# Performance work log

Measured on AMD Instinct MI355X. Metric: run time of the kernel, lower is better.

The kernel has to match this reference:

```python
import jax, jax.numpy as jnp
import numpy as np

S = 7  # adaptive max-pool output size (output_size init kwarg)


def setup_inputs() -> dict:
    key = jax.random.key(0)
    k1, k2, k3, k4, k5, k6 = jax.random.split(key, 6)
    N, C, H, W, R = 4, 256, 50, 50, 256
    images = jax.random.normal(k1, (N, C, H, W), dtype=jnp.float32)
    # Normalized boxes [x1, y1, x2, y2] with strictly positive width/height
    x1 = jax.random.uniform(k2, (R,), minval=0.0, maxval=0.6)
    y1 = jax.random.uniform(k3, (R,), minval=0.0, maxval=0.6)
    bw = jax.random.uniform(k4, (R,), minval=0.1, maxval=0.4)
    bh = jax.random.uniform(k5, (R,), minval=0.1, maxval=0.4)
    rois = jnp.stack([x1, y1, jnp.minimum(x1 + bw, 1.0), jnp.minimum(y1 + bh, 1.0)], axis=1).astype(jnp.float32)
    roi_idx = jax.random.randint(k6, (R,), 0, N, dtype=jnp.int32)
    return {"images": images, "rois": rois, "roi_idx": roi_idx}


def _adaptive_bin_masks(lo, size, n_in):
    # PyTorch adaptive pooling bins for input length `size`, offset by crop start `lo`:
    #   start_i = lo + floor(i*size/S), end_i = lo + ceil((i+1)*size/S)
    i = jnp.arange(S)
    start = lo[:, None] + (i[None, :] * size[:, None]) // S            # [R,S]
    end = lo[:, None] + ((i[None, :] + 1) * size[:, None] + S - 1) // S  # [R,S]
    pos = jnp.arange(n_in)
    return (pos[None, None, :] >= start[..., None]) & (pos[None, None, :] < end[..., None])  # [R,S,n_in]


def reference(images, rois, roi_idx):
    N, C, H, W = images.shape
    x1 = jnp.floor(rois[:, 0] * W).astype(jnp.int32)
    y1 = jnp.floor(rois[:, 1] * H).astype(jnp.int32)
    x2 = jnp.ceil(rois[:, 2] * W).astype(jnp.int32)
    y2 = jnp.ceil(rois[:, 3] * H).astype(jnp.int32)
    mask_w = _adaptive_bin_masks(x1, x2 - x1, W)  # [R,S,W]
    mask_h = _adaptive_bin_masks(y1, y2 - y1, H)  # [R,S,H]
    feats = images[roi_idx]                        # [R,C,H,W] gather per ROI
    neg = jnp.array(-jnp.inf, dtype=images.dtype)
    # masked max over W for each of the S output columns (small fixed loop)
    cols = [jnp.max(jnp.where(mask_w[:, j, None, None, :], feats, neg), axis=-1) for j in range(S)]
    t = jnp.stack(cols, axis=-1)  # [R,C,H,S]
    # masked max over H for each of the S output rows
    rows = [jnp.max(jnp.where(mask_h[:, i, None, :, None], t, neg), axis=2) for i in range(S)]
    return jnp.stack(rows, axis=2)  # [R,C,S,S]
```

## Files before the change

### kernel.cpp

```cpp
#include <hip/hip_runtime.h>
#include <hip/hip_bf16.h>
#include <math.h>


#define S 7
#define NN 4
#define NC 256
#define NH 50
#define NW 50
#define PLANE (NH * NW)
#define MAXD 22
#define PITCH 33
#define PPW 4
#define WPB 4

__global__ __launch_bounds__(256) void roipool_kernel(
    const float* __restrict__ images,
    const float* __restrict__ rois,
    const int* __restrict__ roi_idx,
    float* __restrict__ out,
    int out_size)
{
    __shared__ float lds[WPB][MAXD * PITCH];

    const int lane = threadIdx.x & 63;
    const int wid  = __builtin_amdgcn_readfirstlane((int)(threadIdx.x >> 6));
    const int g    = blockIdx.x * WPB + wid;
    int r          = g >> 6;
    r = min(r, 255);
    const int c0   = (g & 63) * PPW;

    const float rx1 = rois[4 * r + 0];
    const float ry1 = rois[4 * r + 1];
    const float rx2 = rois[4 * r + 2];
    const float ry2 = rois[4 * r + 3];
    int x1 = (int)floorf(rx1 * (float)NW);
    int y1 = (int)floorf(ry1 * (float)NH);
    int x2 = (int)ceilf(rx2 * (float)NW);
    int y2 = (int)ceilf(ry2 * (float)NH);
    x1 = min(max(x1, 0), NW - 1);
    y1 = min(max(y1, 0), NH - 1);
    x2 = min(max(x2, x1 + 1), NW);
    y2 = min(max(y2, y1 + 1), NH);
    const int sw = min(x2 - x1, MAXD);
    const int sh = min(y2 - y1, MAXD);

    int n = roi_idx[r];
    n = min(max(n, 0), NN - 1);

    const int wl = lane & 31;
    const int rh = lane >> 5;
    const int oi = lane / S;
    const int oj = lane % S;

    float* __restrict__ L = lds[wid];

    const int hs = (oi * sh) / S;
    const int he = (oi + 1) * sh / S + (((oi + 1) * sh) % S != 0 ? 1 : 0);
    const int ws = (oj * sw) / S;
    const int we = (oj + 1) * sw / S + (((oj + 1) * sw) % S != 0 ? 1 : 0);

    int ho[4], wo[4];
#pragma unroll
    for (int a = 0; a < 4; ++a) ho[a] = min(hs + a, he - 1) * PITCH;
#pragma unroll
    for (int b = 0; b < 4; ++b) wo[b] = min(ws + b, we - 1);

    for (int k = 0; k < PPW; ++k) {
        const int c = c0 + k;
        const float* __restrict__ base =
            images + ((size_t)(n * NC + c)) * PLANE + y1 * NW + x1;

        for (int t0 = 0; t0 < sh; t0 += 2) {
            const int hh = t0 + rh;
            if (hh < sh && wl < sw) {
                L[hh * PITCH + wl] = base[hh * NW + wl];
            }
        }
        __syncthreads();

        if (lane < S * S) {
            float m = -INFINITY;
#pragma unroll
            for (int a = 0; a < 4; ++a) {
#pragma unroll
                for (int b = 0; b < 4; ++b) {
                    m = fmaxf(m, L[ho[a] + wo[b]]);
                }
            }
            const int oidx = ((r * NC + c) * (S * S)) + lane;
            if (oidx < out_size) out[oidx] = m;
        }
        __syncthreads();
    }
}

extern "C" void kernel_launch(void* const* d_in, const int* in_sizes, int n_in,
                              void* d_out, int out_size, void* d_ws, size_t ws_size,
                              hipStream_t stream) {
    const float* images  = (const float*)d_in[0];
    const float* rois    = (const float*)d_in[1];
    const int*   roi_idx = (const int*)d_in[2];
    float* out = (float*)d_out;

    const int planes = out_size / (S * S);
    const int groups = (planes + PPW - 1) / PPW;
    const int blocks = (groups + WPB - 1) / WPB;
    roipool_kernel<<<blocks, 256, 0, stream>>>(images, rois, roi_idx, out, out_size);
}
```

Before: 88.40 us.

## Map one plane per wave and load fixed-size clamped crop without branches

Each wave now handles a single (ROI, channel) plane instead of four, which multiplies the grid fourfold and removes the per-channel loop with its two barriers per iteration. The crop load is fully unrolled over the maximum height with clamped indices, so every lane issues its loads unconditionally and the loop count no longer depends on the ROI. This gives more memory-level parallelism and occupancy, at the cost of redundant loads of clamped rows and columns and more blocks to launch.

```diff
diff --git a/kernel.cpp b/kernel.cpp
--- a/kernel.cpp
+++ b/kernel.cpp
@@ -11,7 +11,6 @@
 #define PLANE (NH * NW)
 #define MAXD 22
 #define PITCH 33
-#define PPW 4
 #define WPB 4
 
 __global__ __launch_bounds__(256) void roipool_kernel(
@@ -23,12 +22,12 @@
 {
     __shared__ float lds[WPB][MAXD * PITCH];
 
-    const int lane = threadIdx.x & 63;
-    const int wid  = __builtin_amdgcn_readfirstlane((int)(threadIdx.x >> 6));
-    const int g    = blockIdx.x * WPB + wid;
-    int r          = g >> 6;
-    r = min(r, 255);
-    const int c0   = (g & 63) * PPW;
+    const int t     = threadIdx.x;
+    const int wid   = t >> 6;
+    const int lane  = t & 63;
+    const int plane = blockIdx.x * WPB + wid;
+    const int r     = plane >> 8;
+    const int c     = plane & 255;
 
     const float rx1 = rois[4 * r + 0];
     const float ry1 = rois[4 * r + 1];
@@ -48,51 +47,42 @@
     int n = roi_idx[r];
     n = min(max(n, 0), NN - 1);
 
-    const int wl = lane & 31;
-    const int rh = lane >> 5;
-    const int oi = lane / S;
-    const int oj = lane % S;
+    const int wl  = lane & 31;
+    const int rh  = lane >> 5;
+    const int wlc = min(wl, sw - 1);
+    const float* __restrict__ base =
+        images + ((size_t)(n * NC + c)) * PLANE + (y1 * NW + x1) + wlc;
+    float* __restrict__ L = &lds[wid][0];
 
-    float* __restrict__ L = lds[wid];
+#pragma unroll
+    for (int t0 = 0; t0 < MAXD; t0 += 2) {
+        const int hh = t0 + rh;
+        const int hc = min(hh, sh - 1);
+        L[hh * PITCH + wl] = base[hc * NW];
+    }
+    __syncthreads();
 
-    const int hs = (oi * sh) / S;
-    const int he = (oi + 1) * sh / S + (((oi + 1) * sh) % S != 0 ? 1 : 0);
-    const int ws = (oj * sw) / S;
-    const int we = (oj + 1) * sw / S + (((oj + 1) * sw) % S != 0 ? 1 : 0);
+    const int l  = min(lane, S * S - 1);
+    const int i  = l / S;
+    const int j  = l - i * S;
+    const int hs = (i * sh) / S;
+    const int he = ((i + 1) * sh + S - 1) / S;
+    const int ws = (j * sw) / S;
+    const int we = ((j + 1) * sw + S - 1) / S;
 
-    int ho[4], wo[4];
+    float m = -INFINITY;
 #pragma unroll
-    for (int a = 0; a < 4; ++a) ho[a] = min(hs + a, he - 1) * PITCH;
+    for (int a = 0; a < 4; ++a) {
+        const int ha = min(hs + a, he - 1) * PITCH;
 #pragma unroll
-    for (int b = 0; b < 4; ++b) wo[b] = min(ws + b, we - 1);
+        for (int b = 0; b < 4; ++b) {
+            const int wb = min(ws + b, we - 1);
+            m = fmaxf(m, L[ha + wb]);
+        }
+    }
 
-    for (int k = 0; k < PPW; ++k) {
-        const int c = c0 + k;
-        const float* __restrict__ base =
-            images + ((size_t)(n * NC + c)) * PLANE + y1 * NW + x1;
-
-        for (int t0 = 0; t0 < sh; t0 += 2) {
-            const int hh = t0 + rh;
-            if (hh < sh && wl < sw) {
-                L[hh * PITCH + wl] = base[hh * NW + wl];
-            }
-        }
-        __syncthreads();
-
-        if (lane < S * S) {
-            float m = -INFINITY;
-#pragma unroll
-            for (int a = 0; a < 4; ++a) {
-#pragma unroll
-                for (int b = 0; b < 4; ++b) {
-                    m = fmaxf(m, L[ho[a] + wo[b]]);
-                }
-            }
-            const int oidx = ((r * NC + c) * (S * S)) + lane;
-            if (oidx < out_size) out[oidx] = m;
-        }
-        __syncthreads();
-    }
+    const size_t oi = (size_t)plane * (S * S) + lane;
+    if (lane < S * S && oi < (size_t)out_size) out[oi] = m;
 }
 
 extern "C" void kernel_launch(void* const* d_in, const int* in_sizes, int n_in,
@@ -104,7 +94,6 @@
     float* out = (float*)d_out;
 
     const int planes = out_size / (S * S);
-    const int groups = (planes + PPW - 1) / PPW;
-    const int blocks = (groups + WPB - 1) / WPB;
+    const int blocks = (planes + WPB - 1) / WPB;
     roipool_kernel<<<blocks, 256, 0, stream>>>(images, rois, roi_idx, out, out_size);
 }
```

Measured after the change: 81.61 us. 1.08x faster.
